# Kernel optimization log

Hardware: AMD Instinct MI355X
Metric: run time of the kernel (lower is better)

Reference implementation:

```python
import jax, jax.numpy as jnp
import numpy as np

L = 2        # enc_depth
D = 1024     # enc_dim
HS = 1024    # hidden_size
NH = 16      # enc_heads
DH = 64      # dim_head
FF = 4096    # ff_mult * enc_dim
ROT = 32     # rotary dim = min(dim_head, 32)
B, SQ, SK = 64, 128, 512
EPS = 1e-8


def rmsnorm(x, w):
    # torch: x / clamp(||x||_2 * d**-0.5, eps) * w
    norm = jnp.sqrt(jnp.sum(x * x, axis=-1, keepdims=True)) * (x.shape[-1] ** -0.5)
    return x / jnp.maximum(norm, EPS) * w


def rope_freqs(n):
    inv_freq = 1.0 / (10000.0 ** (jnp.arange(0, ROT, 2, dtype=jnp.float32) / ROT))
    f = jnp.arange(n, dtype=jnp.float32)[:, None] * inv_freq[None, :]   # [n, ROT/2]
    return jnp.concatenate([f, f], axis=-1)[None, None]                  # [1,1,n,ROT]


def apply_rope(t, freqs):
    rd = freqs.shape[-1]
    t1, tp = t[..., :rd], t[..., rd:]
    half = rd // 2
    a, b = t1[..., :half], t1[..., half:]
    rot = jnp.concatenate([-b, a], axis=-1)
    t1 = t1 * jnp.cos(freqs) + rot * jnp.sin(freqs)
    return jnp.concatenate([t1, tp], axis=-1)


def attention(x, ctx, Wq, Wk, Wv, Wo, bo, pe_q, pe_k, mask):
    b, n, _ = x.shape
    m = ctx.shape[1]
    q = (x @ Wq).reshape(b, n, NH, DH).transpose(0, 2, 1, 3) * (DH ** -0.5)  # b h n d
    k = (ctx @ Wk).reshape(b, m, NH, DH).transpose(0, 2, 1, 3)
    v = (ctx @ Wv).reshape(b, m, NH, DH).transpose(0, 2, 1, 3)
    q = apply_rope(q, pe_q)
    k = apply_rope(k, pe_k)
    sim = jnp.einsum('bhid,bhjd->bhij', q, k)
    if mask is not None:
        sim = jnp.where(mask[:, None, None, :], sim, -jnp.finfo(sim.dtype).max)
    attn = jax.nn.softmax(sim, axis=-1)
    out = jnp.einsum('bhij,bhjd->bhid', attn, v)
    out = out.transpose(0, 2, 1, 3).reshape(b, n, NH * DH)
    return out @ Wo + bo


def setup_inputs() -> dict:
    key = jax.random.key(0)
    ks = jax.random.split(key, 24)
    s = 0.02
    inp = {
        'x': jax.random.normal(ks[0], (B, SQ, D), jnp.float32),
        'chunked_seq': jax.random.normal(ks[1], (B, SK, HS), jnp.float32),
        'mask': jnp.ones((B, SQ), dtype=bool),
        'attn_norm_w': jnp.ones((L, D), jnp.float32),
        'Wq': jax.random.normal(ks[2], (L, D, NH * DH), jnp.float32) * s,
        'Wk': jax.random.normal(ks[3], (L, D, NH * DH), jnp.float32) * s,
        'Wv': jax.random.normal(ks[4], (L, D, NH * DH), jnp.float32) * s,
        'Wo': jax.random.normal(ks[5], (L, NH * DH, D), jnp.float32) * s,
        'bo': jnp.zeros((L, D), jnp.float32),
        'cross_norm_w': jnp.ones((L, D), jnp.float32),
        'cWq': jax.random.normal(ks[6], (L, D, NH * DH), jnp.float32) * s,
        'cWk': jax.random.normal(ks[7], (HS, NH * DH), jnp.float32) * s if False else jax.random.normal(ks[7], (L, HS, NH * DH), jnp.float32) * s,
        'cWv': jax.random.normal(ks[8], (L, HS, NH * DH), jnp.float32) * s,
        'cWo': jax.random.normal(ks[9], (L, NH * DH, D), jnp.float32) * s,
        'cbo': jnp.zeros((L, D), jnp.float32),
        'ff_norm_w': jnp.ones((L, D), jnp.float32),
        'ff_w1': jax.random.normal(ks[10], (L, D, FF), jnp.float32) * s,
        'ff_b1': jnp.zeros((L, FF), jnp.float32),
        'ff_w2': jax.random.normal(ks[11], (L, FF, D), jnp.float32) * s,
        'ff_b2': jnp.zeros((L, D), jnp.float32),
        'norm_out_w': jnp.ones((D,), jnp.float32),
        'proj_w': jax.random.normal(ks[12], (D, HS), jnp.float32) * s,
        'proj_b': jnp.zeros((HS,), jnp.float32),
    }
    return inp


def reference(x, chunked_seq, mask, attn_norm_w, Wq, Wk, Wv, Wo, bo,
              cross_norm_w, cWq, cWk, cWv, cWo, cbo,
              ff_norm_w, ff_w1, ff_b1, ff_w2, ff_b2,
              norm_out_w, proj_w, proj_b):
    pe_q = rope_freqs(x.shape[-2])
    pe_k = rope_freqs(chunked_seq.shape[-2])
    for l in range(L):
        # PreNorm self-attention (RoPE on both q and k with q_pos_emb)
        h = rmsnorm(x, attn_norm_w[l])
        x = attention(h, h, Wq[l], Wk[l], Wv[l], Wo[l], bo[l], pe_q, pe_q, mask) + x
        # PreNorm cross-attention to chunked_seq (no mask)
        h = rmsnorm(x, cross_norm_w[l])
        x = attention(h, chunked_seq, cWq[l], cWk[l], cWv[l], cWo[l], cbo[l], pe_q, pe_k, None) + x
        # PreNorm feed-forward (exact GELU, as torch nn.GELU default)
        h = rmsnorm(x, ff_norm_w[l])
        x = (jax.nn.gelu(h @ ff_w1[l] + ff_b1[l], approximate=False) @ ff_w2[l] + ff_b2[l]) + x
    x = rmsnorm(x, norm_out_w)
    return x @ proj_w + proj_b
```

## Files before the change

### kernel.cpp

```cpp
#include <hip/hip_runtime.h>
#include <hip/hip_bf16.h>
#include <math.h>

typedef __hip_bfloat16 bf16;
typedef __bf16 bf16x8 __attribute__((ext_vector_type(8)));
typedef float f32x4 __attribute__((ext_vector_type(4)));

#define L_   2
#define D_   1024
#define NH_  16
#define DH_  64
#define FF_  4096
#define B_   64
#define SQ_  128
#define SK_  512
#define MTOK (B_ * SQ_)
#define MCTX (B_ * SK_)

#define GLDS16(gp, lp) __builtin_amdgcn_global_load_lds( \
    (__attribute__((address_space(1))) void*)(gp),        \
    (__attribute__((address_space(3))) void*)(lp), 16, 0, 0)

__global__ __launch_bounds__(256) void transpose_kernel(
    const float* __restrict__ in, bf16* __restrict__ out, int R, int C, float scale)
{
  __shared__ bf16 t[32][33];
  const int bx = blockIdx.x * 32;
  const int by = blockIdx.y * 32;
  const int tid = threadIdx.x;
#pragma unroll
  for (int e = 0; e < 4; ++e) {
    int i = tid + e * 256, rr = i >> 5, cc = i & 31;
    t[rr][cc] = __float2bfloat16(scale * in[(size_t)(by + rr) * C + bx + cc]);
  }
  __syncthreads();
#pragma unroll
  for (int e = 0; e < 4; ++e) {
    int i = tid + e * 256, rr = i >> 5, cc = i & 31;
    out[(size_t)(bx + rr) * R + by + cc] = t[cc][rr];
  }
}

__global__ __launch_bounds__(256) void convert_kernel(
    const float* __restrict__ in, bf16* __restrict__ out)
{
  const size_t i = ((size_t)blockIdx.x * 256 + threadIdx.x) * 8;
  const float4 f0 = *(const float4*)(in + i);
  const float4 f1 = *(const float4*)(in + i + 4);
  bf16x8 v = { (__bf16)f0.x, (__bf16)f0.y, (__bf16)f0.z, (__bf16)f0.w,
               (__bf16)f1.x, (__bf16)f1.y, (__bf16)f1.z, (__bf16)f1.w };
  *(bf16x8*)(out + i) = v;
}

__global__ __launch_bounds__(256) void rmsnorm_kernel(
    const float* __restrict__ x, const float* __restrict__ w, bf16* __restrict__ out)
{
  const int row = blockIdx.x, tid = threadIdx.x;
  const float4 v = ((const float4*)(x + (size_t)row * D_))[tid];
  float ss = v.x * v.x + v.y * v.y + v.z * v.z + v.w * v.w;
#pragma unroll
  for (int m = 1; m < 64; m <<= 1) ss += __shfl_xor(ss, m, 64);
  __shared__ float red[4];
  if ((tid & 63) == 0) red[tid >> 6] = ss;
  __syncthreads();
  const float tot = red[0] + red[1] + red[2] + red[3];
  const float inv = 1.0f / fmaxf(sqrtf(tot * (1.0f / D_)), 1e-8f);
  const float4 wv = ((const float4*)w)[tid];
  bf16* o = out + (size_t)row * D_ + tid * 4;
  o[0] = __float2bfloat16(v.x * inv * wv.x);
  o[1] = __float2bfloat16(v.y * inv * wv.y);
  o[2] = __float2bfloat16(v.z * inv * wv.z);
  o[3] = __float2bfloat16(v.w * inv * wv.w);
}

__global__ __launch_bounds__(256) void rope_kernel(bf16* __restrict__ t, int posmask, int ld)
{
  const int row = blockIdx.x, tid = threadIdx.x;
  const int h = tid >> 4, d = tid & 15;
  const float pos = (float)(row & posmask);
  const float inv_freq = expf(-(float)d * 0.5756462732485115f);
  const float f = pos * inv_freq;
  const float c = cosf(f), s = sinf(f);
  const size_t base = (size_t)row * ld + h * DH_ + d;
  const float a = __bfloat162float(t[base]);
  const float b = __bfloat162float(t[base + 16]);
  t[base]      = __float2bfloat16(a * c - b * s);
  t[base + 16] = __float2bfloat16(b * c + a * s);
}

template <int MODE, int AF32>
__global__ __launch_bounds__(256) void gemm_bt_kernel(
    const void* __restrict__ Ap, const bf16* __restrict__ Bt,
    void* Cout, const float* __restrict__ bias, const float* resid,
    int M, int N, int K)
{
  __shared__ __align__(16) char smem[16384];
  bf16* As = (bf16*)smem;
  bf16* Bs = (bf16*)(smem + 8192);
  const int tid = threadIdx.x;
  const int wave = tid >> 6, lane = tid & 63;
  const int wm = wave >> 1, wn = wave & 1;

  const int npidn = gridDim.x, npidm = gridDim.y;
  const int pid = blockIdx.y * npidn + blockIdx.x;
  const int group_sz = 8 * npidn;
  const int gid = pid / group_sz;
  const int first_m = gid * 8;
  const int gsm = min(npidm - first_m, 8);
  const int pid_m = first_m + (pid % gsm);
  const int pid_n = (pid % group_sz) / gsm;
  const int m0 = pid_m * 128, n0 = pid_n * 128;

  const int r = lane & 15, qd = lane >> 4;
  const int srow = lane >> 2, scol = (lane & 3) * 8;

  f32x4 acc[4][4] = {};

  for (int k0 = 0; k0 < K; k0 += 32) {
#pragma unroll
    for (int t = 0; t < 2; ++t) {
      const int g = wave * 2 + t;
      if (AF32) {
        const float* A32 = (const float*)Ap;
        const float4 f0 = *(const float4*)(A32 + (size_t)(m0 + g * 16 + srow) * K + k0 + scol);
        const float4 f1 = *(const float4*)(A32 + (size_t)(m0 + g * 16 + srow) * K + k0 + scol + 4);
        bf16x8 v = { (__bf16)f0.x, (__bf16)f0.y, (__bf16)f0.z, (__bf16)f0.w,
                     (__bf16)f1.x, (__bf16)f1.y, (__bf16)f1.z, (__bf16)f1.w };
        *(bf16x8*)&As[g * 512 + lane * 8] = v;
      } else {
        const bf16* A16 = (const bf16*)Ap;
        GLDS16(A16 + (size_t)(m0 + g * 16 + srow) * K + k0 + scol, &As[g * 512]);
      }
      GLDS16(Bt + (size_t)(n0 + g * 16 + srow) * K + k0 + scol, &Bs[g * 512]);
    }
    __syncthreads();
    bf16x8 af[4], bfr[4];
#pragma unroll
    for (int i = 0; i < 4; ++i)
      af[i] = *(const bf16x8*)&As[(wm * 64 + i * 16 + r) * 32 + qd * 8];
#pragma unroll
    for (int j = 0; j < 4; ++j)
      bfr[j] = *(const bf16x8*)&Bs[(wn * 64 + j * 16 + r) * 32 + qd * 8];
#pragma unroll
    for (int i = 0; i < 4; ++i)
#pragma unroll
      for (int j = 0; j < 4; ++j)
        acc[i][j] = __builtin_amdgcn_mfma_f32_16x16x32_bf16(af[i], bfr[j], acc[i][j], 0, 0, 0);
    __syncthreads();
  }

  if (MODE == 0 || MODE == 1) {
    bf16* Wb = (bf16*)smem + wave * (16 * 68);
    const int rw = lane >> 2, c0 = (lane & 3) * 8;
#pragma unroll
    for (int i = 0; i < 4; ++i) {
#pragma unroll
      for (int j = 0; j < 4; ++j) {
        const int col = wn * 64 + j * 16 + r;
        const float bv = bias ? bias[n0 + col] : 0.f;
#pragma unroll
        for (int rr = 0; rr < 4; ++rr) {
          float v = acc[i][j][rr] + bv;
          if (MODE == 1) v = 0.5f * v * (1.f + erff(v * 0.70710678118654752f));
          Wb[(qd * 4 + rr) * 68 + j * 16 + r] = __float2bfloat16(v);
        }
      }
      asm volatile("s_waitcnt lgkmcnt(0)" ::: "memory");
      const int row_g = m0 + wm * 64 + i * 16 + rw;
      const bf16x8 v0 = *(const bf16x8*)&Wb[rw * 68 + c0];
      const bf16x8 v1 = *(const bf16x8*)&Wb[rw * 68 + 32 + c0];
      *(bf16x8*)((bf16*)Cout + (size_t)row_g * N + n0 + wn * 64 + c0)      = v0;
      *(bf16x8*)((bf16*)Cout + (size_t)row_g * N + n0 + wn * 64 + 32 + c0) = v1;
      asm volatile("" ::: "memory");
    }
  } else {
#pragma unroll
    for (int i = 0; i < 4; ++i) {
      const int row = m0 + wm * 64 + i * 16 + qd * 4;
#pragma unroll
      for (int j = 0; j < 4; ++j) {
        const int col = n0 + wn * 64 + j * 16 + r;
        const float bv = bias ? bias[col] : 0.f;
#pragma unroll
        for (int rr = 0; rr < 4; ++rr) {
          float v = acc[i][j][rr] + bv;
          const size_t idx = (size_t)(row + rr) * N + col;
          if (MODE == 2) ((float*)Cout)[idx] = v + resid[idx];
          else           ((float*)Cout)[idx] = v;
        }
      }
    }
  }
}

__global__ __launch_bounds__(256) void attn_kernel(
    const bf16* __restrict__ Q, const bf16* __restrict__ Kg,
    const bf16* __restrict__ Vg, bf16* __restrict__ Out,
    int nk, int ldq, int ldkv)
{
  __shared__ __align__(16) bf16 Qs[128 * 64];
  __shared__ __align__(16) bf16 Ks[64 * 64];
  __shared__ __align__(16) bf16 Vt[64 * 64];
  __shared__ __align__(16) bf16 Ps[128 * 64];
  const int tid = threadIdx.x;
  const int wave = tid >> 6, lane = tid & 63;
  const int b = blockIdx.x >> 4, h = blockIdx.x & 15;
  const int r = lane & 15, qd = lane >> 4;
  const int srow = lane >> 3;
  const int scol = ((lane & 7) ^ srow) * 8;

#pragma unroll
  for (int t = 0; t < 4; ++t) {
    const int g = wave * 4 + t;
    GLDS16(Q + (size_t)(b * SQ_ + g * 8 + srow) * ldq + h * DH_ + scol, &Qs[g * 512]);
  }

  float mrow[2][4], lrow[2][4];
  f32x4 Oacc[2][4] = {};
#pragma unroll
  for (int i = 0; i < 2; ++i)
#pragma unroll
    for (int rr = 0; rr < 4; ++rr) { mrow[i][rr] = -1e30f; lrow[i][rr] = 0.f; }

  for (int kt = 0; kt < nk; kt += 64) {
#pragma unroll
    for (int t = 0; t < 2; ++t) {
      const int g = wave * 2 + t;
      GLDS16(Kg + (size_t)(b * nk + kt + g * 8 + srow) * ldkv + h * DH_ + scol, &Ks[g * 512]);
    }
#pragma unroll
    for (int c = 0; c < 2; ++c) {
      const int chunk = c * 256 + tid;
      const int key = chunk >> 3, d0 = (chunk & 7) * 8;
      const uint4 pv = *(const uint4*)(Vg + (size_t)(b * nk + kt + key) * ldkv + h * DH_ + d0);
      const unsigned short* pu = (const unsigned short*)&pv;
      const int s0 = key >> 3, k7 = key & 7;
#pragma unroll
      for (int t2 = 0; t2 < 8; ++t2) {
        const int row = d0 + t2;
        ((unsigned short*)Vt)[row * 64 + ((s0 ^ (row & 7)) << 3) + k7] = pu[t2];
      }
    }
    __syncthreads();

    f32x4 S[2][4] = {};
#pragma unroll
    for (int ks = 0; ks < 2; ++ks) {
      const int sl = ((ks * 4 + qd) ^ (r & 7)) * 8;
      bf16x8 aq[2], bk[4];
#pragma unroll
      for (int i = 0; i < 2; ++i)
        aq[i] = *(const bf16x8*)&Qs[(wave * 32 + i * 16 + r) * 64 + sl];
#pragma unroll
      for (int j = 0; j < 4; ++j)
        bk[j] = *(const bf16x8*)&Ks[(j * 16 + r) * 64 + sl];
#pragma unroll
      for (int i = 0; i < 2; ++i)
#pragma unroll
        for (int j = 0; j < 4; ++j)
          S[i][j] = __builtin_amdgcn_mfma_f32_16x16x32_bf16(aq[i], bk[j], S[i][j], 0, 0, 0);
    }

#pragma unroll
    for (int i = 0; i < 2; ++i) {
#pragma unroll
      for (int rr = 0; rr < 4; ++rr) {
        float mx = fmaxf(fmaxf(S[i][0][rr], S[i][1][rr]), fmaxf(S[i][2][rr], S[i][3][rr]));
#pragma unroll
        for (int mm = 1; mm < 16; mm <<= 1) mx = fmaxf(mx, __shfl_xor(mx, mm, 64));
        const float mnew = fmaxf(mrow[i][rr], mx);
        const float alpha = __expf(mrow[i][rr] - mnew);
        mrow[i][rr] = mnew;
        const int prow = wave * 32 + i * 16 + qd * 4 + rr;
        const int pr7 = prow & 7;
        float rs = 0.f;
#pragma unroll
        for (int j = 0; j < 4; ++j) {
          const float p = __expf(S[i][j][rr] - mnew);
          rs += p;
          Ps[prow * 64 + (((j * 2 + (r >> 3)) ^ pr7) << 3) + (r & 7)] = __float2bfloat16(p);
        }
#pragma unroll
        for (int mm = 1; mm < 16; mm <<= 1) rs += __shfl_xor(rs, mm, 64);
        lrow[i][rr] = lrow[i][rr] * alpha + rs;
#pragma unroll
        for (int jd = 0; jd < 4; ++jd) Oacc[i][jd][rr] *= alpha;
      }
    }
    __syncthreads();

#pragma unroll
    for (int ks = 0; ks < 2; ++ks) {
      const int sl = ((ks * 4 + qd) ^ (r & 7)) * 8;
      bf16x8 ap[2], bv[4];
#pragma unroll
      for (int i = 0; i < 2; ++i)
        ap[i] = *(const bf16x8*)&Ps[(wave * 32 + i * 16 + r) * 64 + sl];
#pragma unroll
      for (int jd = 0; jd < 4; ++jd)
        bv[jd] = *(const bf16x8*)&Vt[(jd * 16 + r) * 64 + sl];
#pragma unroll
      for (int i = 0; i < 2; ++i)
#pragma unroll
        for (int jd = 0; jd < 4; ++jd)
          Oacc[i][jd] = __builtin_amdgcn_mfma_f32_16x16x32_bf16(ap[i], bv[jd], Oacc[i][jd], 0, 0, 0);
    }
    __syncthreads();
  }

#pragma unroll
  for (int i = 0; i < 2; ++i) {
    const int rowl = wave * 32 + i * 16 + qd * 4;
#pragma unroll
    for (int jd = 0; jd < 4; ++jd) {
      const int col = h * DH_ + jd * 16 + r;
#pragma unroll
      for (int rr = 0; rr < 4; ++rr)
        Out[(size_t)(b * SQ_ + rowl + rr) * D_ + col] =
            __float2bfloat16(Oacc[i][jd][rr] / lrow[i][rr]);
    }
  }
}

extern "C" void kernel_launch(void* const* d_in, const int* in_sizes, int n_in,
                              void* d_out, int out_size, void* d_ws, size_t ws_size,
                              hipStream_t stream)
{
  (void)in_sizes; (void)n_in; (void)out_size;
  const float* x_in         = (const float*)d_in[0];
  const float* ctx          = (const float*)d_in[1];
  const float* attn_norm_w  = (const float*)d_in[3];
  const float* Wq           = (const float*)d_in[4];
  const float* Wk           = (const float*)d_in[5];
  const float* Wv           = (const float*)d_in[6];
  const float* Wo           = (const float*)d_in[7];
  const float* bo           = (const float*)d_in[8];
  const float* cross_norm_w = (const float*)d_in[9];
  const float* cWq          = (const float*)d_in[10];
  const float* cWk          = (const float*)d_in[11];
  const float* cWv          = (const float*)d_in[12];
  const float* cWo          = (const float*)d_in[13];
  const float* cbo          = (const float*)d_in[14];
  const float* ff_norm_w    = (const float*)d_in[15];
  const float* ff_w1        = (const float*)d_in[16];
  const float* ff_b1        = (const float*)d_in[17];
  const float* ff_w2        = (const float*)d_in[18];
  const float* ff_b2        = (const float*)d_in[19];
  const float* norm_out_w   = (const float*)d_in[20];
  const float* proj_w       = (const float*)d_in[21];
  const float* proj_b       = (const float*)d_in[22];

  char* ws = (char*)d_ws;
  size_t off = 0;
  auto carve = [&](size_t bytes) -> void* {
    void* p = ws + off;
    off += (bytes + 255) & ~(size_t)255;
    return p;
  };
  const size_t DD = (size_t)D_ * D_;
  bf16*  Wt  = (bf16*)carve((size_t)FF_ * D_ * 2);
  float* xf  = (float*)carve((size_t)MTOK * D_ * 4);
  bf16*  hb  = (bf16*)carve((size_t)MTOK * D_ * 2);
  bf16*  ao  = hb;
  char*  big = (char*)carve((size_t)144 * 1024 * 1024);
  bf16*  qkvb = (bf16*)big;
  bf16*  qb   = (bf16*)big;
  bf16*  kvb  = (bf16*)(big + (size_t)16 * 1024 * 1024);
  bf16*  gbuf = (bf16*)big;
  bf16*  ctxb = (bf16*)carve((size_t)MCTX * D_ * 2);
  const bool ctx16 = (ws_size >= off);

  auto T = [&](const float* src, bf16* dst, int R, int C, float scale = 1.0f) {
    transpose_kernel<<<dim3(C / 32, R / 32), 256, 0, stream>>>(src, dst, R, C, scale);
  };
  auto G0 = [&](const bf16* A, bf16* C, int M, int N, int K) {
    gemm_bt_kernel<0, 0><<<dim3(N / 128, M / 128), 256, 0, stream>>>(
        (const void*)A, Wt, (void*)C, nullptr, nullptr, M, N, K);
  };
  auto G0f = [&](const float* A, bf16* C, int M, int N, int K) {
    gemm_bt_kernel<0, 1><<<dim3(N / 128, M / 128), 256, 0, stream>>>(
        (const void*)A, Wt, (void*)C, nullptr, nullptr, M, N, K);
  };
  auto G1 = [&](const bf16* A, bf16* C, const float* bias, int M, int N, int K) {
    gemm_bt_kernel<1, 0><<<dim3(N / 128, M / 128), 256, 0, stream>>>(
        (const void*)A, Wt, (void*)C, bias, nullptr, M, N, K);
  };
  auto G2 = [&](const bf16* A, const float* bias, const float* resid, int M, int N, int K) {
    gemm_bt_kernel<2, 0><<<dim3(N / 128, M / 128), 256, 0, stream>>>(
        (const void*)A, Wt, (void*)xf, bias, resid, M, N, K);
  };
  auto G3 = [&](const bf16* A, float* C, const float* bias, int M, int N, int K) {
    gemm_bt_kernel<3, 0><<<dim3(N / 128, M / 128), 256, 0, stream>>>(
        (const void*)A, Wt, (void*)C, bias, nullptr, M, N, K);
  };

  if (ctx16)
    convert_kernel<<<(MCTX * D_) / (256 * 8), 256, 0, stream>>>(ctx, ctxb);

  for (int l = 0; l < L_; ++l) {
    const size_t o1 = (size_t)l * DD;
    const size_t o4 = (size_t)l * D_ * FF_;
    const float* res0 = (l == 0) ? x_in : xf;
    rmsnorm_kernel<<<MTOK, 256, 0, stream>>>(res0, attn_norm_w + l * D_, hb);
    T(Wq + o1, Wt,          D_, D_, 0.125f);
    T(Wk + o1, Wt + DD,     D_, D_);
    T(Wv + o1, Wt + 2 * DD, D_, D_);
    G0(hb, qkvb, MTOK, 3 * D_, D_);
    rope_kernel<<<MTOK, 256, 0, stream>>>(qkvb,        SQ_ - 1, 3 * D_);
    rope_kernel<<<MTOK, 256, 0, stream>>>(qkvb + D_,   SQ_ - 1, 3 * D_);
    attn_kernel<<<B_ * NH_, 256, 0, stream>>>(qkvb, qkvb + D_, qkvb + 2 * D_, ao,
                                              SQ_, 3 * D_, 3 * D_);
    T(Wo + o1, Wt, D_, D_);
    G2(ao, bo + l * D_, res0, MTOK, D_, D_);
    rmsnorm_kernel<<<MTOK, 256, 0, stream>>>(xf, cross_norm_w + l * D_, hb);
    T(cWq + o1, Wt, D_, D_, 0.125f);
    G0(hb, qb, MTOK, D_, D_);
    T(cWk + o1, Wt,      D_, D_);
    T(cWv + o1, Wt + DD, D_, D_);
    if (ctx16) G0(ctxb, kvb, MCTX, 2 * D_, D_);
    else       G0f(ctx, kvb, MCTX, 2 * D_, D_);
    rope_kernel<<<MTOK, 256, 0, stream>>>(qb,  SQ_ - 1, D_);
    rope_kernel<<<MCTX, 256, 0, stream>>>(kvb, SK_ - 1, 2 * D_);
    attn_kernel<<<B_ * NH_, 256, 0, stream>>>(qb, kvb, kvb + D_, ao, SK_, D_, 2 * D_);
    T(cWo + o1, Wt, D_, D_);
    G2(ao, cbo + l * D_, xf, MTOK, D_, D_);
    rmsnorm_kernel<<<MTOK, 256, 0, stream>>>(xf, ff_norm_w + l * D_, hb);
    T(ff_w1 + o4, Wt, D_, FF_);
    G1(hb, gbuf, ff_b1 + l * FF_, MTOK, FF_, D_);
    T(ff_w2 + o4, Wt, FF_, D_);
    G2(gbuf, ff_b2 + l * D_, xf, MTOK, D_, FF_);
  }
  rmsnorm_kernel<<<MTOK, 256, 0, stream>>>(xf, norm_out_w, hb);
  T(proj_w, Wt, D_, D_);
  G3(hb, (float*)d_out, proj_b, MTOK, D_, D_);
}
```

Baseline: 2.115 ms.

## Add 256x256-tile pipelined GEMM kernel for large projections and FFN

Adds a new 512-thread GEMM kernel with 256x256 output tiles, a double-buffered LDS pipeline fed by direct global-to-LDS loads, swizzled LDS layout, explicit vmcnt waits, priority hints and block remapping. It replaces the 128x128 GEMM for the fused QKV projection, the context KV projection and both FFN GEMMs. The larger tiles are meant to raise arithmetic intensity and reuse per LDS load. In exchange there are fewer workgroups and higher register and LDS pressure, which could leave the GPU underfilled on the smaller N=1024 FFN2 GEMM.

```diff
diff --git a/kernel.cpp b/kernel.cpp
--- a/kernel.cpp
+++ b/kernel.cpp
@@ -187,6 +187,149 @@
           const size_t idx = (size_t)(row + rr) * N + col;
           if (MODE == 2) ((float*)Cout)[idx] = v + resid[idx];
           else           ((float*)Cout)[idx] = v;
+        }
+      }
+    }
+  }
+}
+
+#define VM8 asm volatile("s_waitcnt vmcnt(8)" ::: "memory")
+#define VM4 asm volatile("s_waitcnt vmcnt(4)" ::: "memory")
+#define VM0 asm volatile("s_waitcnt vmcnt(0)" ::: "memory")
+#define NOPST (void)0
+
+#define PHASE256(BUF, KK, H, STAGE_STMT, WAIT_STMT) {                                   \
+  bf16x8 af[4], bv[4];                                                                  \
+  const int ab_ = ((BUF) * 2 + (KK)) * 8192;                                            \
+  const int bb_ = 32768 + ((BUF) * 2 + (KK)) * 8192;                                    \
+  _Pragma("unroll") for (int i2 = 0; i2 < 4; ++i2) {                                    \
+    const int rl = wm * 128 + (H) * 64 + i2 * 16 + r;                                   \
+    af[i2] = *(const bf16x8*)&sm[ab_ + rl * 32 + ((qd ^ ((rl >> 1) & 3)) << 3)];        \
+  }                                                                                     \
+  _Pragma("unroll") for (int j = 0; j < 4; ++j) {                                       \
+    const int rl = wn * 64 + j * 16 + r;                                                \
+    bv[j] = *(const bf16x8*)&sm[bb_ + rl * 32 + ((qd ^ ((rl >> 1) & 3)) << 3)];         \
+  }                                                                                     \
+  STAGE_STMT;                                                                           \
+  __builtin_amdgcn_s_barrier();                                                         \
+  asm volatile("s_waitcnt lgkmcnt(0)" ::: "memory");                                    \
+  __builtin_amdgcn_sched_barrier(0);                                                    \
+  __builtin_amdgcn_s_setprio(1);                                                        \
+  _Pragma("unroll") for (int i2 = 0; i2 < 4; ++i2)                                      \
+    _Pragma("unroll") for (int j = 0; j < 4; ++j)                                       \
+      acc[(H) * 4 + i2][j] =                                                            \
+          __builtin_amdgcn_mfma_f32_16x16x32_bf16(af[i2], bv[j], acc[(H) * 4 + i2][j],  \
+                                                  0, 0, 0);                             \
+  __builtin_amdgcn_s_setprio(0);                                                        \
+  WAIT_STMT;                                                                            \
+  __builtin_amdgcn_s_barrier();                                                         \
+  __builtin_amdgcn_sched_barrier(0);                                                    \
+}
+
+template <int MODE>
+__global__ __launch_bounds__(512, 2) void gemm256_kernel(
+    const bf16* __restrict__ A, const bf16* __restrict__ Bt,
+    void* Cout, const float* __restrict__ bias, const float* __restrict__ resid,
+    int M, int N, int K)
+{
+  __shared__ __align__(16) bf16 sm[65536];
+  const int tid = threadIdx.x;
+  const int wave = tid >> 6, lane = tid & 63;
+  const int wm = wave >> 2, wn = wave & 3;
+  const int r = lane & 15, qd = lane >> 4;
+
+  const int nbn = N >> 8;
+  const int nwg = (M >> 8) * nbn;
+  int pid = blockIdx.x;
+  if ((nwg & 7) == 0) pid = (pid & 7) * (nwg >> 3) + (pid >> 3);
+  const int m0 = (pid / nbn) << 8, n0 = (pid % nbn) << 8;
+
+  const int srow = lane >> 2, ssl = lane & 3;
+  auto stage = [&](const bf16* src, int row0, int kbase, int slab) {
+    const int ra = wave * 32 + srow;
+    GLDS16(src + (size_t)(row0 + ra) * K + kbase + ((ssl ^ ((ra >> 1) & 3)) << 3),
+           &sm[slab + wave * 1024]);
+    const int rb = ra + 16;
+    GLDS16(src + (size_t)(row0 + rb) * K + kbase + ((ssl ^ ((rb >> 1) & 3)) << 3),
+           &sm[slab + wave * 1024 + 512]);
+  };
+  auto AOF = [](int buf, int kk) { return (buf * 2 + kk) * 8192; };
+  auto BOF = [](int buf, int kk) { return 32768 + (buf * 2 + kk) * 8192; };
+
+  f32x4 acc[8][4] = {};
+
+  stage(A,  m0, 0,  AOF(0, 0));
+  stage(Bt, n0, 0,  BOF(0, 0));
+  stage(A,  m0, 32, AOF(0, 1));
+  stage(Bt, n0, 32, BOF(0, 1));
+  stage(A,  m0, 64, AOF(1, 0));
+  stage(Bt, n0, 64, BOF(1, 0));
+  VM8;
+  __builtin_amdgcn_s_barrier();
+  __builtin_amdgcn_sched_barrier(0);
+
+  const int NT = K >> 6;
+  int buf = 0;
+  for (int t = 0; t + 2 < NT; ++t) {
+    const int o = buf;
+    PHASE256(o, 0, 0, stage(A,  m0, (t + 1) * 64 + 32, AOF(o ^ 1, 1)), NOPST);
+    PHASE256(o, 0, 1, stage(Bt, n0, (t + 1) * 64 + 32, BOF(o ^ 1, 1)), VM8);
+    PHASE256(o, 1, 0, stage(A,  m0, (t + 2) * 64,      AOF(o, 0)),     NOPST);
+    PHASE256(o, 1, 1, stage(Bt, n0, (t + 2) * 64,      BOF(o, 0)),     VM8);
+    buf ^= 1;
+  }
+  {
+    const int o = buf, t = NT - 2;
+    PHASE256(o, 0, 0, stage(A,  m0, (t + 1) * 64 + 32, AOF(o ^ 1, 1)), NOPST);
+    PHASE256(o, 0, 1, stage(Bt, n0, (t + 1) * 64 + 32, BOF(o ^ 1, 1)), VM8);
+    PHASE256(o, 1, 0, NOPST, NOPST);
+    PHASE256(o, 1, 1, NOPST, VM4);
+    buf ^= 1;
+  }
+  {
+    const int o = buf;
+    PHASE256(o, 0, 0, NOPST, NOPST);
+    PHASE256(o, 0, 1, NOPST, VM0);
+    PHASE256(o, 1, 0, NOPST, NOPST);
+    PHASE256(o, 1, 1, NOPST, NOPST);
+  }
+
+  if (MODE <= 1) {
+    bf16* Wb = sm + wave * (16 * 68);
+    const int rw = lane >> 2, c0 = (lane & 3) * 8;
+#pragma unroll
+    for (int i = 0; i < 8; ++i) {
+#pragma unroll
+      for (int j = 0; j < 4; ++j) {
+        const int col = wn * 64 + j * 16 + r;
+        const float bvs = bias ? bias[n0 + col] : 0.f;
+#pragma unroll
+        for (int rr = 0; rr < 4; ++rr) {
+          float v = acc[i][j][rr] + bvs;
+          if (MODE == 1) v = 0.5f * v * (1.f + erff(v * 0.70710678118654752f));
+          Wb[(qd * 4 + rr) * 68 + j * 16 + r] = __float2bfloat16(v);
+        }
+      }
+      asm volatile("s_waitcnt lgkmcnt(0)" ::: "memory");
+      const int row_g = m0 + wm * 128 + i * 16 + rw;
+      const bf16x8 v0 = *(const bf16x8*)&Wb[rw * 68 + c0];
+      const bf16x8 v1 = *(const bf16x8*)&Wb[rw * 68 + 32 + c0];
+      *(bf16x8*)((bf16*)Cout + (size_t)row_g * N + n0 + wn * 64 + c0)      = v0;
+      *(bf16x8*)((bf16*)Cout + (size_t)row_g * N + n0 + wn * 64 + 32 + c0) = v1;
+      asm volatile("" ::: "memory");
+    }
+  } else {
+#pragma unroll
+    for (int i = 0; i < 8; ++i) {
+      const int row = m0 + wm * 128 + i * 16 + qd * 4;
+#pragma unroll
+      for (int j = 0; j < 4; ++j) {
+        const int col = n0 + wn * 64 + j * 16 + r;
+        const float bv = bias ? bias[col] : 0.f;
+#pragma unroll
+        for (int rr = 0; rr < 4; ++rr) {
+          const size_t idx = (size_t)(row + rr) * N + col;
+          ((float*)Cout)[idx] = acc[i][j][rr] + bv + (resid ? resid[idx] : 0.f);
         }
       }
     }
@@ -381,10 +524,6 @@
     gemm_bt_kernel<0, 1><<<dim3(N / 128, M / 128), 256, 0, stream>>>(
         (const void*)A, Wt, (void*)C, nullptr, nullptr, M, N, K);
   };
-  auto G1 = [&](const bf16* A, bf16* C, const float* bias, int M, int N, int K) {
-    gemm_bt_kernel<1, 0><<<dim3(N / 128, M / 128), 256, 0, stream>>>(
-        (const void*)A, Wt, (void*)C, bias, nullptr, M, N, K);
-  };
   auto G2 = [&](const bf16* A, const float* bias, const float* resid, int M, int N, int K) {
     gemm_bt_kernel<2, 0><<<dim3(N / 128, M / 128), 256, 0, stream>>>(
         (const void*)A, Wt, (void*)xf, bias, resid, M, N, K);
@@ -392,6 +531,18 @@
   auto G3 = [&](const bf16* A, float* C, const float* bias, int M, int N, int K) {
     gemm_bt_kernel<3, 0><<<dim3(N / 128, M / 128), 256, 0, stream>>>(
         (const void*)A, Wt, (void*)C, bias, nullptr, M, N, K);
+  };
+  auto H0 = [&](const bf16* A, bf16* C, int M, int N, int K) {
+    gemm256_kernel<0><<<dim3((M / 256) * (N / 256)), 512, 0, stream>>>(
+        A, Wt, (void*)C, nullptr, nullptr, M, N, K);
+  };
+  auto H1 = [&](const bf16* A, bf16* C, const float* bias, int M, int N, int K) {
+    gemm256_kernel<1><<<dim3((M / 256) * (N / 256)), 512, 0, stream>>>(
+        A, Wt, (void*)C, bias, nullptr, M, N, K);
+  };
+  auto H2 = [&](const bf16* A, const float* bias, const float* resid, int M, int N, int K) {
+    gemm256_kernel<2><<<dim3((M / 256) * (N / 256)), 512, 0, stream>>>(
+        A, Wt, (void*)xf, bias, resid, M, N, K);
   };
 
   if (ctx16)
@@ -405,9 +556,9 @@
     T(Wq + o1, Wt,          D_, D_, 0.125f);
     T(Wk + o1, Wt + DD,     D_, D_);
     T(Wv + o1, Wt + 2 * DD, D_, D_);
-    G0(hb, qkvb, MTOK, 3 * D_, D_);
-    rope_kernel<<<MTOK, 256, 0, stream>>>(qkvb,        SQ_ - 1, 3 * D_);
-    rope_kernel<<<MTOK, 256, 0, stream>>>(qkvb + D_,   SQ_ - 1, 3 * D_);
+    H0(hb, qkvb, MTOK, 3 * D_, D_);
+    rope_kernel<<<MTOK, 256, 0, stream>>>(qkvb,      SQ_ - 1, 3 * D_);
+    rope_kernel<<<MTOK, 256, 0, stream>>>(qkvb + D_, SQ_ - 1, 3 * D_);
     attn_kernel<<<B_ * NH_, 256, 0, stream>>>(qkvb, qkvb + D_, qkvb + 2 * D_, ao,
                                               SQ_, 3 * D_, 3 * D_);
     T(Wo + o1, Wt, D_, D_);
@@ -417,7 +568,7 @@
     G0(hb, qb, MTOK, D_, D_);
     T(cWk + o1, Wt,      D_, D_);
     T(cWv + o1, Wt + DD, D_, D_);
-    if (ctx16) G0(ctxb, kvb, MCTX, 2 * D_, D_);
+    if (ctx16) H0(ctxb, kvb, MCTX, 2 * D_, D_);
     else       G0f(ctx, kvb, MCTX, 2 * D_, D_);
     rope_kernel<<<MTOK, 256, 0, stream>>>(qb,  SQ_ - 1, D_);
     rope_kernel<<<MCTX, 256, 0, stream>>>(kvb, SK_ - 1, 2 * D_);
@@ -426,9 +577,9 @@
     G2(ao, cbo + l * D_, xf, MTOK, D_, D_);
     rmsnorm_kernel<<<MTOK, 256, 0, stream>>>(xf, ff_norm_w + l * D_, hb);
     T(ff_w1 + o4, Wt, D_, FF_);
-    G1(hb, gbuf, ff_b1 + l * FF_, MTOK, FF_, D_);
+    H1(hb, gbuf, ff_b1 + l * FF_, MTOK, FF_, D_);
     T(ff_w2 + o4, Wt, FF_, D_);
-    G2(gbuf, ff_b2 + l * D_, xf, MTOK, D_, FF_);
+    H2(gbuf, ff_b2 + l * D_, xf, MTOK, D_, FF_);
   }
   rmsnorm_kernel<<<MTOK, 256, 0, stream>>>(xf, norm_out_w, hb);
   T(proj_w, Wt, D_, D_);
```

Measured after the change: 2.265 ms. +7.1%, slower.
